# Performance work log

Hardware: AMD Instinct MI355X
Metric: run time of the kernel (lower is better)

Reference implementation:

```python
import jax, jax.numpy as jnp
import numpy as np

NEG_BIG = -1e9

def setup_inputs() -> dict:
    key = jax.random.key(0)
    kq, kk, kv, kwq, kwk, kwv, km = jax.random.split(key, 7)
    B, S, d = 16, 1024, 512
    Q = jax.random.normal(kq, (B, S, d), dtype=jnp.float32)
    K = jax.random.normal(kk, (B, S, d), dtype=jnp.float32)
    V = jax.random.normal(kv, (B, S, d), dtype=jnp.float32)
    # nn.Linear weights [d, d]; torch applies x @ W.T
    WQ = jax.random.normal(kwq, (d, d), dtype=jnp.float32) / np.sqrt(d)
    WK = jax.random.normal(kwk, (d, d), dtype=jnp.float32) / np.sqrt(d)
    WV = jax.random.normal(kwv, (d, d), dtype=jnp.float32) / np.sqrt(d)
    mask = jax.random.randint(km, (B, S), 0, 2, dtype=jnp.int32)
    return {"Q": Q, "K": K, "V": V, "WQ": WQ, "WK": WK, "WV": WV, "mask": mask}


def reference(Q, K, V, WQ, WK, WV, mask):
    d = Q.shape[-1]
    q = jnp.einsum('bsd,ed->bse', Q, WQ)
    k = jnp.einsum('bsd,ed->bse', K, WK)
    v = jnp.einsum('bsd,ed->bse', V, WV)
    scores = jnp.einsum('bqd,bkd->bqk', q, k) / jnp.sqrt(jnp.float32(d))
    attn = jax.nn.softmax(scores, axis=-1)
    # Faithful to original: mask applied AFTER softmax with -1e9 fill
    m = mask[:, None, :]  # [B,1,S] broadcast over query dim
    attn = jnp.where(m == 0, jnp.float32(NEG_BIG), attn)
    out = jnp.einsum('bqk,bkd->bqd', attn, v)
    return (out, attn)
```

## Files before the change

kernel.cpp:

```cpp
#include <hip/hip_runtime.h>
#include <hip/hip_bf16.h>

typedef float f32x4 __attribute__((ext_vector_type(4)));
typedef __bf16 bf16x8 __attribute__((ext_vector_type(8)));
typedef unsigned short u16x8 __attribute__((ext_vector_type(8)));
typedef unsigned short u16x4 __attribute__((ext_vector_type(4)));
typedef int i32x4 __attribute__((ext_vector_type(4)));

#define NEG_BIG_F (-1000000000.0f)
#define SCALE_F 0.044194173824159216f

__device__ __forceinline__ unsigned short f2bf(float f) {
  unsigned int u = __float_as_uint(f);
  u += 0x7FFFu + ((u >> 16) & 1u);
  return (unsigned short)(u >> 16);
}

__device__ __forceinline__ u16x8 cvt8(f32x4 a, f32x4 b) {
  u16x8 r;
  r[0] = f2bf(a[0]); r[1] = f2bf(a[1]); r[2] = f2bf(a[2]); r[3] = f2bf(a[3]);
  r[4] = f2bf(b[0]); r[5] = f2bf(b[1]); r[6] = f2bf(b[2]); r[7] = f2bf(b[3]);
  return r;
}

__device__ __forceinline__ bf16x8 u2b(u16x8 u) {
  union { u16x8 u; bf16x8 b; } c; c.u = u; return c.b;
}

__device__ __forceinline__ void gload16(const void* g, char* l) {
  __builtin_amdgcn_global_load_lds(
      (const __attribute__((address_space(1))) unsigned int*)g,
      (__attribute__((address_space(3))) unsigned int*)l, 16, 0, 0);
}

__global__ __launch_bounds__(256) void cvtW(
    const float* __restrict__ w0, const float* __restrict__ w1,
    const float* __restrict__ w2, unsigned short* __restrict__ out)
{
  const float* src = blockIdx.z == 0 ? w0 : (blockIdx.z == 1 ? w1 : w2);
  unsigned short* dst = out + (size_t)blockIdx.z * 262144;
  const int i = (blockIdx.x * 256 + threadIdx.x) * 8;
  f32x4 a = *(const f32x4*)(src + i);
  f32x4 b = *(const f32x4*)(src + i + 4);
  *(u16x8*)&dst[i] = cvt8(a, b);
}

__global__ __launch_bounds__(256) void proj3(
    const float* __restrict__ Q, const float* __restrict__ Kx,
    const float* __restrict__ V, const unsigned short* __restrict__ wb,
    unsigned short* __restrict__ qb, unsigned short* __restrict__ kb,
    unsigned short* __restrict__ vt)
{
  __shared__ __align__(16) float          Af[2][128][32];
  __shared__ __align__(16) unsigned short Bs[2][128][32];

  const int tid = threadIdx.x;
  const int z = blockIdx.z;
  const float* X = (z == 0) ? Q : (z == 1 ? Kx : V);
  const unsigned short* W = wb + (size_t)z * 262144;
  const int m0 = blockIdx.x * 128, n0 = blockIdx.y * 128;
  const int lane = tid & 63, wave = tid >> 6;
  const int wr = (wave >> 1) * 64, wc = (wave & 1) * 64;
  const int fr = lane & 15, fq = lane >> 4;

  f32x4 acc[4][4] = {};

  const float* gA[4]; char* lA[4];
  #pragma unroll
  for (int i = 0; i < 4; i++) {
    const int c = tid + 256 * i, row = c >> 3, slot = c & 7;
    gA[i] = X + (size_t)(m0 + row) * 512 + ((slot ^ (row & 7)) * 4);
    lA[i] = (char*)&Af[0][0][0] + c * 16;
  }
  const int c1 = 256 + tid;
  const int br0 = tid >> 2, br1 = c1 >> 2;
  const unsigned short* gB0 = W + (size_t)(n0 + br0) * 512 + ((tid & 3) ^ ((br0 >> 1) & 3)) * 8;
  const unsigned short* gB1 = W + (size_t)(n0 + br1) * 512 + ((c1 & 3) ^ ((br1 >> 1) & 3)) * 8;
  char* lB0 = (char*)&Bs[0][0][0] + tid * 16;
  char* lB1 = (char*)&Bs[0][0][0] + c1 * 16;

  #pragma unroll
  for (int i = 0; i < 4; i++) gload16(gA[i], lA[i]);
  gload16(gB0, lB0); gload16(gB1, lB1);
  __syncthreads();

  int cur = 0;
  for (int kt = 0; kt < 512; kt += 32) {
    const int nb = cur ^ 1;
    if (kt + 32 < 512) {
      #pragma unroll
      for (int i = 0; i < 4; i++) gload16(gA[i] + kt + 32, lA[i] + nb * 16384);
      gload16(gB0 + kt + 32, lB0 + nb * 8192);
      gload16(gB1 + kt + 32, lB1 + nb * 8192);
    }
    bf16x8 af[4], bv[4];
    #pragma unroll
    for (int t = 0; t < 4; t++) {
      const int arow = wr + t * 16 + fr;
      const int s0 = (fq * 2) ^ (arow & 7), s1 = (fq * 2 + 1) ^ (arow & 7);
      f32x4 lo = *(const f32x4*)&Af[cur][arow][s0 * 4];
      f32x4 hi = *(const f32x4*)&Af[cur][arow][s1 * 4];
      af[t] = u2b(cvt8(lo, hi));
      const int brow = wc + t * 16 + fr;
      bv[t] = *(const bf16x8*)&Bs[cur][brow][(fq ^ ((brow >> 1) & 3)) * 8];
    }
    #pragma unroll
    for (int mt = 0; mt < 4; mt++)
      #pragma unroll
      for (int nt = 0; nt < 4; nt++)
        acc[mt][nt] = __builtin_amdgcn_mfma_f32_16x16x32_bf16(af[mt], bv[nt], acc[mt][nt], 0, 0, 0);
    __syncthreads();
    cur = nb;
  }

  if (z == 2) {
    #pragma unroll
    for (int mt = 0; mt < 4; mt++)
      #pragma unroll
      for (int nt = 0; nt < 4; nt++)
        #pragma unroll
        for (int rr = 0; rr < 4; rr++) {
          const int m = m0 + wr + mt * 16 + fq * 4 + rr;
          const int n = n0 + wc + nt * 16 + fr;
          vt[((size_t)(m >> 10) * 512 + n) * 1024 + (m & 1023)] = f2bf(acc[mt][nt][rr]);
        }
  } else {
    unsigned short* Y = (z == 0) ? qb : kb;
    #pragma unroll
    for (int mt = 0; mt < 4; mt++)
      #pragma unroll
      for (int nt = 0; nt < 4; nt++)
        #pragma unroll
        for (int rr = 0; rr < 4; rr++) {
          const int m = m0 + wr + mt * 16 + fq * 4 + rr;
          const int n = n0 + wc + nt * 16 + fr;
          Y[(size_t)m * 512 + n] = f2bf(acc[mt][nt][rr]);
        }
  }
}

__global__ __launch_bounds__(256) void score_gemm(
    const unsigned short* __restrict__ qb, const unsigned short* __restrict__ kb,
    float* __restrict__ attn, float* __restrict__ partial)
{
  __shared__ __align__(16) unsigned short As[2][128][32];
  __shared__ __align__(16) unsigned short Bs[2][128][32];

  const int tid = threadIdx.x, z = blockIdx.z;
  const int m0 = blockIdx.x * 128, n0 = blockIdx.y * 128;
  const int lane = tid & 63, wave = tid >> 6;
  const int wr = (wave >> 1) * 64, wc = (wave & 1) * 64;
  const int fr = lane & 15, fq = lane >> 4;

  f32x4 acc[4][4] = {};

  const int c1 = 256 + tid;
  const int br0 = tid >> 2, br1 = c1 >> 2;
  const int sw0 = ((tid & 3) ^ ((br0 >> 1) & 3)) * 8;
  const int sw1 = ((c1 & 3) ^ ((br1 >> 1) & 3)) * 8;
  const unsigned short* gA0 = qb + ((size_t)z * 1024 + m0 + br0) * 512 + sw0;
  const unsigned short* gA1 = qb + ((size_t)z * 1024 + m0 + br1) * 512 + sw1;
  const unsigned short* gB0 = kb + ((size_t)z * 1024 + n0 + br0) * 512 + sw0;
  const unsigned short* gB1 = kb + ((size_t)z * 1024 + n0 + br1) * 512 + sw1;
  char* lA0 = (char*)&As[0][0][0] + tid * 16;
  char* lA1 = (char*)&As[0][0][0] + c1 * 16;
  char* lB0 = (char*)&Bs[0][0][0] + tid * 16;
  char* lB1 = (char*)&Bs[0][0][0] + c1 * 16;

  gload16(gA0, lA0); gload16(gA1, lA1);
  gload16(gB0, lB0); gload16(gB1, lB1);
  __syncthreads();

  int cur = 0;
  for (int kt = 0; kt < 512; kt += 32) {
    const int nb = cur ^ 1;
    if (kt + 32 < 512) {
      gload16(gA0 + kt + 32, lA0 + nb * 8192);
      gload16(gA1 + kt + 32, lA1 + nb * 8192);
      gload16(gB0 + kt + 32, lB0 + nb * 8192);
      gload16(gB1 + kt + 32, lB1 + nb * 8192);
    }
    bf16x8 af[4], bv[4];
    #pragma unroll
    for (int t = 0; t < 4; t++) {
      const int arow = wr + t * 16 + fr;
      const int brow = wc + t * 16 + fr;
      af[t] = *(const bf16x8*)&As[cur][arow][(fq ^ ((arow >> 1) & 3)) * 8];
      bv[t] = *(const bf16x8*)&Bs[cur][brow][(fq ^ ((brow >> 1) & 3)) * 8];
    }
    #pragma unroll
    for (int mt = 0; mt < 4; mt++)
      #pragma unroll
      for (int nt = 0; nt < 4; nt++)
        acc[mt][nt] = __builtin_amdgcn_mfma_f32_16x16x32_bf16(af[mt], bv[nt], acc[mt][nt], 0, 0, 0);
    __syncthreads();
    cur = nb;
  }

  float* Cb = attn + (size_t)z * 1024 * 1024;
  const int slot = blockIdx.y * 2 + (wave & 1);
  #pragma unroll
  for (int mt = 0; mt < 4; mt++) {
    #pragma unroll
    for (int rr = 0; rr < 4; rr++) {
      const int m = m0 + wr + mt * 16 + fq * 4 + rr;
      float e = 0.f;
      #pragma unroll
      for (int nt = 0; nt < 4; nt++) {
        const float sv = acc[mt][nt][rr] * SCALE_F;
        Cb[(size_t)m * 1024 + n0 + wc + nt * 16 + fr] = sv;
        e += __expf(sv);
      }
      e += __shfl_xor(e, 1); e += __shfl_xor(e, 2);
      e += __shfl_xor(e, 4); e += __shfl_xor(e, 8);
      if (fr == 0)
        partial[(size_t)slot * 16384 + z * 1024 + m] = e;
    }
  }
}

__global__ __launch_bounds__(256) void rs_inv(
    const float* __restrict__ partial, float* __restrict__ inv)
{
  const int i = blockIdx.x * 256 + threadIdx.x;
  float s = 0.f;
  #pragma unroll
  for (int p = 0; p < 16; p++) s += partial[(size_t)p * 16384 + i];
  inv[i] = 1.0f / s;
}

__global__ __launch_bounds__(512) void pv_gemm(
    float* __restrict__ attn, const unsigned short* __restrict__ vt,
    const float* __restrict__ inv, const int* __restrict__ mask,
    float* __restrict__ out)
{
  __shared__ __align__(16) unsigned short As[2][64][40];
  __shared__ __align__(16) unsigned short Bs[2][512][32];

  const int tid = threadIdx.x;
  const int bz = blockIdx.z, m0 = blockIdx.x * 64;
  const int lane = tid & 63, wave = tid >> 6;
  const int n0 = wave * 64;
  const int fr = lane & 15, fq = lane >> 4;

  f32x4 acc[4][4] = {};

  const int arow = tid >> 3, acol = (tid & 7) * 4;
  float* arp = attn + ((size_t)bz * 1024 + m0 + arow) * 1024 + acol;
  const float vinv = inv[bz * 1024 + m0 + arow];
  const int* mrow = mask + bz * 1024 + acol;

  const unsigned short* gB[4];
  char* lB[4];
  #pragma unroll
  for (int r = 0; r < 4; r++) {
    const int c = r * 512 + tid;
    const int row = c >> 2;
    gB[r] = vt + ((size_t)bz * 512 + row) * 1024 + ((c & 3) ^ ((row >> 1) & 3)) * 8;
    lB[r] = (char*)&Bs[0][0][0] + c * 16;
  }

  {
    f32x4 s = *(const f32x4*)(arp);
    i32x4 mv = *(const i32x4*)(mrow);
    f32x4 p;
    p[0] = mv[0] ? __expf(s[0]) * vinv : NEG_BIG_F;
    p[1] = mv[1] ? __expf(s[1]) * vinv : NEG_BIG_F;
    p[2] = mv[2] ? __expf(s[2]) * vinv : NEG_BIG_F;
    p[3] = mv[3] ? __expf(s[3]) * vinv : NEG_BIG_F;
    *(f32x4*)(arp) = p;
    u16x4 h;
    h[0] = f2bf(p[0]); h[1] = f2bf(p[1]); h[2] = f2bf(p[2]); h[3] = f2bf(p[3]);
    *(u16x4*)&As[0][arow][acol] = h;
    #pragma unroll
    for (int r = 0; r < 4; r++) gload16(gB[r], lB[r]);
  }
  __syncthreads();

  int cur = 0;
  for (int kt = 0; kt < 1024; kt += 32) {
    const int nb = cur ^ 1;
    f32x4 s; i32x4 mv;
    const bool more = (kt + 32) < 1024;
    if (more) {
      s = *(const f32x4*)(arp + kt + 32);
      mv = *(const i32x4*)(mrow + kt + 32);
      #pragma unroll
      for (int r = 0; r < 4; r++) gload16(gB[r] + kt + 32, lB[r] + nb * 32768);
    }

    bf16x8 af[4], bv[4];
    #pragma unroll
    for (int t = 0; t < 4; t++) {
      af[t] = *(const bf16x8*)&As[cur][t * 16 + fr][fq * 8];
      const int brow = n0 + t * 16 + fr;
      bv[t] = *(const bf16x8*)&Bs[cur][brow][(fq ^ ((brow >> 1) & 3)) * 8];
    }
    #pragma unroll
    for (int mt = 0; mt < 4; mt++)
      #pragma unroll
      for (int nt = 0; nt < 4; nt++)
        acc[mt][nt] = __builtin_amdgcn_mfma_f32_16x16x32_bf16(af[mt], bv[nt], acc[mt][nt], 0, 0, 0);

    if (more) {
      f32x4 p;
      p[0] = mv[0] ? __expf(s[0]) * vinv : NEG_BIG_F;
      p[1] = mv[1] ? __expf(s[1]) * vinv : NEG_BIG_F;
      p[2] = mv[2] ? __expf(s[2]) * vinv : NEG_BIG_F;
      p[3] = mv[3] ? __expf(s[3]) * vinv : NEG_BIG_F;
      *(f32x4*)(arp + kt + 32) = p;
      u16x4 h;
      h[0] = f2bf(p[0]); h[1] = f2bf(p[1]); h[2] = f2bf(p[2]); h[3] = f2bf(p[3]);
      *(u16x4*)&As[nb][arow][acol] = h;
    }
    __syncthreads();
    cur = nb;
  }

  #pragma unroll
  for (int mt = 0; mt < 4; mt++)
    #pragma unroll
    for (int nt = 0; nt < 4; nt++)
      #pragma unroll
      for (int rr = 0; rr < 4; rr++)
        out[((size_t)bz * 1024 + m0 + mt * 16 + fq * 4 + rr) * 512 + n0 + nt * 16 + fr] =
            acc[mt][nt][rr];
}

extern "C" void kernel_launch(void* const* d_in, const int* in_sizes, int n_in,
                              void* d_out, int out_size, void* d_ws, size_t ws_size,
                              hipStream_t stream)
{
  const float* Q  = (const float*)d_in[0];
  const float* Kx = (const float*)d_in[1];
  const float* V  = (const float*)d_in[2];
  const float* WQ = (const float*)d_in[3];
  const float* WK = (const float*)d_in[4];
  const float* WV = (const float*)d_in[5];
  const int* mask = (const int*)d_in[6];

  const int B = 16, S = 1024, D = 512;
  float* out_f  = (float*)d_out;
  float* attn_f = out_f + (size_t)B * S * D;

  unsigned short* qb = (unsigned short*)d_ws;
  unsigned short* kb = qb + (size_t)B * S * D;
  unsigned short* vt = kb + (size_t)B * S * D;
  unsigned short* wb = vt + (size_t)B * S * D;
  float* partial = (float*)(wb + 786432);
  float* inv = partial + 262144;

  cvtW<<<dim3(128, 1, 3), 256, 0, stream>>>(WQ, WK, WV, wb);
  proj3<<<dim3(128, 4, 3), 256, 0, stream>>>(Q, Kx, V, wb, qb, kb, vt);
  score_gemm<<<dim3(8, 8, 16), 256, 0, stream>>>(qb, kb, attn_f, partial);
  rs_inv<<<dim3(64), 256, 0, stream>>>(partial, inv);
  pv_gemm<<<dim3(16, 1, 16), 512, 0, stream>>>(attn_f, vt, inv, mask, out_f);
}
```

Before: 169.1 us.

## Enlarge projection and score GEMM tiles, split V projection to emit V^T directly

The combined projection kernel is split in two. A Q/K projection kernel uses 256x256 tiles with 512 threads; it prefetches the fp32 activations into registers and converts them to bf16 once before the LDS store, instead of every wave re-converting fp32 from LDS. A separate V projection computes W_V·V^T per batch, so the transposed bf16 V is written with coalesced stores instead of scattered ones. The score GEMM moves to 256x256 tiles with explicit waitcnt/barrier pipelining, which raises data reuse per LDS load. The trade-off is higher register and LDS pressure and fewer, larger blocks, which may hurt latency hiding.

```diff
diff --git a/kernel.cpp b/kernel.cpp
--- a/kernel.cpp
+++ b/kernel.cpp
@@ -45,176 +45,285 @@
   *(u16x8*)&dst[i] = cvt8(a, b);
 }
 
-__global__ __launch_bounds__(256) void proj3(
+__global__ __launch_bounds__(512, 2) void projqk(
     const float* __restrict__ Q, const float* __restrict__ Kx,
-    const float* __restrict__ V, const unsigned short* __restrict__ wb,
-    unsigned short* __restrict__ qb, unsigned short* __restrict__ kb,
-    unsigned short* __restrict__ vt)
-{
-  __shared__ __align__(16) float          Af[2][128][32];
-  __shared__ __align__(16) unsigned short Bs[2][128][32];
-
-  const int tid = threadIdx.x;
-  const int z = blockIdx.z;
-  const float* X = (z == 0) ? Q : (z == 1 ? Kx : V);
+    const unsigned short* __restrict__ wb,
+    unsigned short* __restrict__ qb, unsigned short* __restrict__ kb)
+{
+  __shared__ __align__(16) unsigned short As[2][256][32];
+  __shared__ __align__(16) unsigned short Bs[2][256][32];
+
+  const int tid = threadIdx.x, z = blockIdx.z;
+  const float* X = z ? Kx : Q;
   const unsigned short* W = wb + (size_t)z * 262144;
-  const int m0 = blockIdx.x * 128, n0 = blockIdx.y * 128;
+  unsigned short* Y = z ? kb : qb;
+  const int m0 = blockIdx.x * 256, n0 = blockIdx.y * 256;
   const int lane = tid & 63, wave = tid >> 6;
-  const int wr = (wave >> 1) * 64, wc = (wave & 1) * 64;
+  const int wr = (wave >> 2) * 128, wc = (wave & 3) * 64;
   const int fr = lane & 15, fq = lane >> 4;
 
-  f32x4 acc[4][4] = {};
-
-  const float* gA[4]; char* lA[4];
-  #pragma unroll
-  for (int i = 0; i < 4; i++) {
-    const int c = tid + 256 * i, row = c >> 3, slot = c & 7;
-    gA[i] = X + (size_t)(m0 + row) * 512 + ((slot ^ (row & 7)) * 4);
-    lA[i] = (char*)&Af[0][0][0] + c * 16;
-  }
-  const int c1 = 256 + tid;
-  const int br0 = tid >> 2, br1 = c1 >> 2;
-  const unsigned short* gB0 = W + (size_t)(n0 + br0) * 512 + ((tid & 3) ^ ((br0 >> 1) & 3)) * 8;
-  const unsigned short* gB1 = W + (size_t)(n0 + br1) * 512 + ((c1 & 3) ^ ((br1 >> 1) & 3)) * 8;
-  char* lB0 = (char*)&Bs[0][0][0] + tid * 16;
-  char* lB1 = (char*)&Bs[0][0][0] + c1 * 16;
-
-  #pragma unroll
-  for (int i = 0; i < 4; i++) gload16(gA[i], lA[i]);
-  gload16(gB0, lB0); gload16(gB1, lB1);
-  __syncthreads();
+  f32x4 acc[8][4] = {};
+
+  int arow_s[2], aswz_s[2];
+  const float* gAs[2];
+  #pragma unroll
+  for (int i = 0; i < 2; i++) {
+    const int c = tid + 512 * i;
+    arow_s[i] = c >> 2;
+    aswz_s[i] = ((c & 3) ^ ((arow_s[i] >> 1) & 3)) * 8;
+    gAs[i] = X + (size_t)(m0 + arow_s[i]) * 512 + (c & 3) * 8;
+  }
+  const unsigned short* gB[2]; char* lB[2];
+  #pragma unroll
+  for (int i = 0; i < 2; i++) {
+    const int c = tid + 512 * i, row = c >> 2, slot = c & 3;
+    gB[i] = W + (size_t)(n0 + row) * 512 + (slot ^ ((row >> 1) & 3)) * 8;
+    lB[i] = (char*)&Bs[0][0][0] + c * 16;
+  }
+
+  f32x4 pa[2][2];
+  #pragma unroll
+  for (int i = 0; i < 2; i++) {
+    pa[i][0] = *(const f32x4*)(gAs[i]);
+    pa[i][1] = *(const f32x4*)(gAs[i] + 4);
+  }
+  #pragma unroll
+  for (int i = 0; i < 2; i++) gload16(gB[i], lB[i]);
+  #pragma unroll
+  for (int i = 0; i < 2; i++)
+    *(u16x8*)&As[0][arow_s[i]][aswz_s[i]] = cvt8(pa[i][0], pa[i][1]);
 
   int cur = 0;
   for (int kt = 0; kt < 512; kt += 32) {
     const int nb = cur ^ 1;
-    if (kt + 32 < 512) {
-      #pragma unroll
-      for (int i = 0; i < 4; i++) gload16(gA[i] + kt + 32, lA[i] + nb * 16384);
-      gload16(gB0 + kt + 32, lB0 + nb * 8192);
-      gload16(gB1 + kt + 32, lB1 + nb * 8192);
-    }
-    bf16x8 af[4], bv[4];
-    #pragma unroll
-    for (int t = 0; t < 4; t++) {
-      const int arow = wr + t * 16 + fr;
-      const int s0 = (fq * 2) ^ (arow & 7), s1 = (fq * 2 + 1) ^ (arow & 7);
-      f32x4 lo = *(const f32x4*)&Af[cur][arow][s0 * 4];
-      f32x4 hi = *(const f32x4*)&Af[cur][arow][s1 * 4];
-      af[t] = u2b(cvt8(lo, hi));
-      const int brow = wc + t * 16 + fr;
-      bv[t] = *(const bf16x8*)&Bs[cur][brow][(fq ^ ((brow >> 1) & 3)) * 8];
-    }
-    #pragma unroll
-    for (int mt = 0; mt < 4; mt++)
-      #pragma unroll
-      for (int nt = 0; nt < 4; nt++)
-        acc[mt][nt] = __builtin_amdgcn_mfma_f32_16x16x32_bf16(af[mt], bv[nt], acc[mt][nt], 0, 0, 0);
-    __syncthreads();
+    if (kt < 480) {
+      #pragma unroll
+      for (int i = 0; i < 2; i++) {
+        pa[i][0] = *(const f32x4*)(gAs[i] + kt + 32);
+        pa[i][1] = *(const f32x4*)(gAs[i] + kt + 36);
+      }
+      #pragma unroll
+      for (int i = 0; i < 2; i++) gload16(gB[i] + kt + 32, lB[i] + nb * 16384);
+      asm volatile("s_waitcnt vmcnt(6) lgkmcnt(0)" ::: "memory");
+    } else {
+      asm volatile("s_waitcnt vmcnt(0) lgkmcnt(0)" ::: "memory");
+    }
+    __builtin_amdgcn_sched_barrier(0);
+    __builtin_amdgcn_s_barrier();
+
+    bf16x8 bv[4];
+    #pragma unroll
+    for (int nf = 0; nf < 4; nf++) {
+      const int br = wc + nf * 16 + fr;
+      bv[nf] = *(const bf16x8*)&Bs[cur][br][(fq ^ ((br >> 1) & 3)) * 8];
+    }
+    #pragma unroll
+    for (int mf = 0; mf < 8; mf++) {
+      const int ar = wr + mf * 16 + fr;
+      bf16x8 av = *(const bf16x8*)&As[cur][ar][(fq ^ ((ar >> 1) & 3)) * 8];
+      #pragma unroll
+      for (int nf = 0; nf < 4; nf++)
+        acc[mf][nf] = __builtin_amdgcn_mfma_f32_16x16x32_bf16(av, bv[nf], acc[mf][nf], 0, 0, 0);
+    }
+
+    if (kt < 480) {
+      #pragma unroll
+      for (int i = 0; i < 2; i++)
+        *(u16x8*)&As[nb][arow_s[i]][aswz_s[i]] = cvt8(pa[i][0], pa[i][1]);
+    }
+    __builtin_amdgcn_s_barrier();
     cur = nb;
   }
 
-  if (z == 2) {
-    #pragma unroll
-    for (int mt = 0; mt < 4; mt++)
-      #pragma unroll
-      for (int nt = 0; nt < 4; nt++)
-        #pragma unroll
-        for (int rr = 0; rr < 4; rr++) {
-          const int m = m0 + wr + mt * 16 + fq * 4 + rr;
-          const int n = n0 + wc + nt * 16 + fr;
-          vt[((size_t)(m >> 10) * 512 + n) * 1024 + (m & 1023)] = f2bf(acc[mt][nt][rr]);
-        }
-  } else {
-    unsigned short* Y = (z == 0) ? qb : kb;
-    #pragma unroll
-    for (int mt = 0; mt < 4; mt++)
-      #pragma unroll
-      for (int nt = 0; nt < 4; nt++)
-        #pragma unroll
-        for (int rr = 0; rr < 4; rr++) {
-          const int m = m0 + wr + mt * 16 + fq * 4 + rr;
-          const int n = n0 + wc + nt * 16 + fr;
-          Y[(size_t)m * 512 + n] = f2bf(acc[mt][nt][rr]);
-        }
-  }
-}
-
-__global__ __launch_bounds__(256) void score_gemm(
-    const unsigned short* __restrict__ qb, const unsigned short* __restrict__ kb,
-    float* __restrict__ attn, float* __restrict__ partial)
+  #pragma unroll
+  for (int mf = 0; mf < 8; mf++)
+    #pragma unroll
+    for (int nf = 0; nf < 4; nf++)
+      #pragma unroll
+      for (int rr = 0; rr < 4; rr++) {
+        const int m = m0 + wr + mf * 16 + fq * 4 + rr;
+        const int n = n0 + wc + nf * 16 + fr;
+        Y[(size_t)m * 512 + n] = f2bf(acc[mf][nf][rr]);
+      }
+}
+
+__global__ __launch_bounds__(512, 2) void projv(
+    const float* __restrict__ V, const unsigned short* __restrict__ wv,
+    unsigned short* __restrict__ vt)
 {
   __shared__ __align__(16) unsigned short As[2][128][32];
-  __shared__ __align__(16) unsigned short Bs[2][128][32];
-
-  const int tid = threadIdx.x, z = blockIdx.z;
-  const int m0 = blockIdx.x * 128, n0 = blockIdx.y * 128;
+  __shared__ __align__(16) unsigned short Bs[2][256][32];
+
+  const int tid = threadIdx.x;
+  const int m0 = blockIdx.x * 128, n0 = blockIdx.y * 256, b = blockIdx.z;
   const int lane = tid & 63, wave = tid >> 6;
-  const int wr = (wave >> 1) * 64, wc = (wave & 1) * 64;
+  const int wr = (wave >> 2) * 64, wc = (wave & 3) * 64;
   const int fr = lane & 15, fq = lane >> 4;
 
   f32x4 acc[4][4] = {};
 
-  const int c1 = 256 + tid;
-  const int br0 = tid >> 2, br1 = c1 >> 2;
-  const int sw0 = ((tid & 3) ^ ((br0 >> 1) & 3)) * 8;
-  const int sw1 = ((c1 & 3) ^ ((br1 >> 1) & 3)) * 8;
-  const unsigned short* gA0 = qb + ((size_t)z * 1024 + m0 + br0) * 512 + sw0;
-  const unsigned short* gA1 = qb + ((size_t)z * 1024 + m0 + br1) * 512 + sw1;
-  const unsigned short* gB0 = kb + ((size_t)z * 1024 + n0 + br0) * 512 + sw0;
-  const unsigned short* gB1 = kb + ((size_t)z * 1024 + n0 + br1) * 512 + sw1;
-  char* lA0 = (char*)&As[0][0][0] + tid * 16;
-  char* lA1 = (char*)&As[0][0][0] + c1 * 16;
-  char* lB0 = (char*)&Bs[0][0][0] + tid * 16;
-  char* lB1 = (char*)&Bs[0][0][0] + c1 * 16;
-
-  gload16(gA0, lA0); gload16(gA1, lA1);
-  gload16(gB0, lB0); gload16(gB1, lB1);
-  __syncthreads();
+  const int ar_s = tid >> 2, aslot = tid & 3;
+  const unsigned short* gA = wv + (size_t)(m0 + ar_s) * 512 + (aslot ^ ((ar_s >> 1) & 3)) * 8;
+  char* lA = (char*)&As[0][0][0] + tid * 16;
+
+  int brow_s[2], bswz_s[2];
+  const float* gBs[2];
+  #pragma unroll
+  for (int i = 0; i < 2; i++) {
+    const int c = tid + 512 * i;
+    brow_s[i] = c >> 2;
+    bswz_s[i] = ((c & 3) ^ ((brow_s[i] >> 1) & 3)) * 8;
+    gBs[i] = V + ((size_t)b * 1024 + n0 + brow_s[i]) * 512 + (c & 3) * 8;
+  }
+
+  f32x4 pb[2][2];
+  #pragma unroll
+  for (int i = 0; i < 2; i++) {
+    pb[i][0] = *(const f32x4*)(gBs[i]);
+    pb[i][1] = *(const f32x4*)(gBs[i] + 4);
+  }
+  gload16(gA, lA);
+  #pragma unroll
+  for (int i = 0; i < 2; i++)
+    *(u16x8*)&Bs[0][brow_s[i]][bswz_s[i]] = cvt8(pb[i][0], pb[i][1]);
 
   int cur = 0;
   for (int kt = 0; kt < 512; kt += 32) {
     const int nb = cur ^ 1;
-    if (kt + 32 < 512) {
-      gload16(gA0 + kt + 32, lA0 + nb * 8192);
-      gload16(gA1 + kt + 32, lA1 + nb * 8192);
-      gload16(gB0 + kt + 32, lB0 + nb * 8192);
-      gload16(gB1 + kt + 32, lB1 + nb * 8192);
-    }
-    bf16x8 af[4], bv[4];
-    #pragma unroll
-    for (int t = 0; t < 4; t++) {
-      const int arow = wr + t * 16 + fr;
-      const int brow = wc + t * 16 + fr;
-      af[t] = *(const bf16x8*)&As[cur][arow][(fq ^ ((arow >> 1) & 3)) * 8];
-      bv[t] = *(const bf16x8*)&Bs[cur][brow][(fq ^ ((brow >> 1) & 3)) * 8];
-    }
-    #pragma unroll
-    for (int mt = 0; mt < 4; mt++)
-      #pragma unroll
-      for (int nt = 0; nt < 4; nt++)
-        acc[mt][nt] = __builtin_amdgcn_mfma_f32_16x16x32_bf16(af[mt], bv[nt], acc[mt][nt], 0, 0, 0);
-    __syncthreads();
+    if (kt < 480) {
+      #pragma unroll
+      for (int i = 0; i < 2; i++) {
+        pb[i][0] = *(const f32x4*)(gBs[i] + kt + 32);
+        pb[i][1] = *(const f32x4*)(gBs[i] + kt + 36);
+      }
+      gload16(gA + kt + 32, lA + nb * 8192);
+      asm volatile("s_waitcnt vmcnt(5) lgkmcnt(0)" ::: "memory");
+    } else {
+      asm volatile("s_waitcnt vmcnt(0) lgkmcnt(0)" ::: "memory");
+    }
+    __builtin_amdgcn_sched_barrier(0);
+    __builtin_amdgcn_s_barrier();
+
+    bf16x8 av[4], bv[4];
+    #pragma unroll
+    for (int mf = 0; mf < 4; mf++) {
+      const int ar = wr + mf * 16 + fr;
+      av[mf] = *(const bf16x8*)&As[cur][ar][(fq ^ ((ar >> 1) & 3)) * 8];
+    }
+    #pragma unroll
+    for (int nf = 0; nf < 4; nf++) {
+      const int br = wc + nf * 16 + fr;
+      bv[nf] = *(const bf16x8*)&Bs[cur][br][(fq ^ ((br >> 1) & 3)) * 8];
+    }
+    #pragma unroll
+    for (int mf = 0; mf < 4; mf++)
+      #pragma unroll
+      for (int nf = 0; nf < 4; nf++)
+        acc[mf][nf] = __builtin_amdgcn_mfma_f32_16x16x32_bf16(av[mf], bv[nf], acc[mf][nf], 0, 0, 0);
+
+    if (kt < 480) {
+      #pragma unroll
+      for (int i = 0; i < 2; i++)
+        *(u16x8*)&Bs[nb][brow_s[i]][bswz_s[i]] = cvt8(pb[i][0], pb[i][1]);
+    }
+    __builtin_amdgcn_s_barrier();
     cur = nb;
   }
 
-  float* Cb = attn + (size_t)z * 1024 * 1024;
-  const int slot = blockIdx.y * 2 + (wave & 1);
-  #pragma unroll
-  for (int mt = 0; mt < 4; mt++) {
+  #pragma unroll
+  for (int mf = 0; mf < 4; mf++)
+    #pragma unroll
+    for (int nf = 0; nf < 4; nf++)
+      #pragma unroll
+      for (int rr = 0; rr < 4; rr++) {
+        const int e = m0 + wr + mf * 16 + fq * 4 + rr;
+        const int s = n0 + wc + nf * 16 + fr;
+        vt[((size_t)b * 512 + e) * 1024 + s] = f2bf(acc[mf][nf][rr]);
+      }
+}
+
+__global__ __launch_bounds__(512, 2) void score256(
+    const unsigned short* __restrict__ qb, const unsigned short* __restrict__ kb,
+    float* __restrict__ attn, float* __restrict__ partial)
+{
+  __shared__ __align__(16) unsigned short As[2][256][32];
+  __shared__ __align__(16) unsigned short Bs[2][256][32];
+
+  const int tid = threadIdx.x, bz = blockIdx.z;
+  const int m0 = blockIdx.x * 256, n0 = blockIdx.y * 256;
+  const int lane = tid & 63, wave = tid >> 6;
+  const int wr = (wave >> 2) * 128, wc = (wave & 3) * 64;
+  const int fr = lane & 15, fq = lane >> 4;
+
+  f32x4 acc[8][4] = {};
+
+  const unsigned short* gA[2]; char* lA[2];
+  const unsigned short* gB[2]; char* lB[2];
+  #pragma unroll
+  for (int i = 0; i < 2; i++) {
+    const int c = tid + 512 * i, row = c >> 2, slot = c & 3;
+    const int sw = (slot ^ ((row >> 1) & 3)) * 8;
+    gA[i] = qb + ((size_t)bz * 1024 + m0 + row) * 512 + sw;
+    gB[i] = kb + ((size_t)bz * 1024 + n0 + row) * 512 + sw;
+    lA[i] = (char*)&As[0][0][0] + c * 16;
+    lB[i] = (char*)&Bs[0][0][0] + c * 16;
+  }
+
+  #pragma unroll
+  for (int i = 0; i < 2; i++) { gload16(gA[i], lA[i]); gload16(gB[i], lB[i]); }
+
+  int cur = 0;
+  for (int kt = 0; kt < 512; kt += 32) {
+    const int nb = cur ^ 1;
+    if (kt < 480) {
+      #pragma unroll
+      for (int i = 0; i < 2; i++) {
+        gload16(gA[i] + kt + 32, lA[i] + nb * 16384);
+        gload16(gB[i] + kt + 32, lB[i] + nb * 16384);
+      }
+      asm volatile("s_waitcnt vmcnt(4) lgkmcnt(0)" ::: "memory");
+    } else {
+      asm volatile("s_waitcnt vmcnt(0) lgkmcnt(0)" ::: "memory");
+    }
+    __builtin_amdgcn_sched_barrier(0);
+    __builtin_amdgcn_s_barrier();
+
+    bf16x8 bv[4];
+    #pragma unroll
+    for (int nf = 0; nf < 4; nf++) {
+      const int br = wc + nf * 16 + fr;
+      bv[nf] = *(const bf16x8*)&Bs[cur][br][(fq ^ ((br >> 1) & 3)) * 8];
+    }
+    #pragma unroll
+    for (int mf = 0; mf < 8; mf++) {
+      const int ar = wr + mf * 16 + fr;
+      bf16x8 av = *(const bf16x8*)&As[cur][ar][(fq ^ ((ar >> 1) & 3)) * 8];
+      #pragma unroll
+      for (int nf = 0; nf < 4; nf++)
+        acc[mf][nf] = __builtin_amdgcn_mfma_f32_16x16x32_bf16(av, bv[nf], acc[mf][nf], 0, 0, 0);
+    }
+    __builtin_amdgcn_s_barrier();
+    cur = nb;
+  }
+
+  float* Cb = attn + (size_t)bz * 1024 * 1024;
+  const int slot = blockIdx.y * 4 + (wave & 3);
+  #pragma unroll
+  for (int mf = 0; mf < 8; mf++) {
     #pragma unroll
     for (int rr = 0; rr < 4; rr++) {
-      const int m = m0 + wr + mt * 16 + fq * 4 + rr;
+      const int m = m0 + wr + mf * 16 + fq * 4 + rr;
       float e = 0.f;
       #pragma unroll
-      for (int nt = 0; nt < 4; nt++) {
-        const float sv = acc[mt][nt][rr] * SCALE_F;
-        Cb[(size_t)m * 1024 + n0 + wc + nt * 16 + fr] = sv;
+      for (int nf = 0; nf < 4; nf++) {
+        const float sv = acc[mf][nf][rr] * SCALE_F;
+        Cb[(size_t)m * 1024 + n0 + wc + nf * 16 + fr] = sv;
         e += __expf(sv);
       }
       e += __shfl_xor(e, 1); e += __shfl_xor(e, 2);
       e += __shfl_xor(e, 4); e += __shfl_xor(e, 8);
       if (fr == 0)
-        partial[(size_t)slot * 16384 + z * 1024 + m] = e;
+        partial[(size_t)slot * 16384 + bz * 1024 + m] = e;
     }
   }
 }
@@ -351,8 +460,9 @@
   float* inv = partial + 262144;
 
   cvtW<<<dim3(128, 1, 3), 256, 0, stream>>>(WQ, WK, WV, wb);
-  proj3<<<dim3(128, 4, 3), 256, 0, stream>>>(Q, Kx, V, wb, qb, kb, vt);
-  score_gemm<<<dim3(8, 8, 16), 256, 0, stream>>>(qb, kb, attn_f, partial);
+  projqk<<<dim3(64, 2, 2), 512, 0, stream>>>(Q, Kx, wb, qb, kb);
+  projv<<<dim3(4, 4, 16), 512, 0, stream>>>(V, wb + 524288, vt);
+  score256<<<dim3(4, 4, 16), 512, 0, stream>>>(qb, kb, attn_f, partial);
   rs_inv<<<dim3(64), 256, 0, stream>>>(partial, inv);
   pv_gemm<<<dim3(16, 1, 16), 512, 0, stream>>>(attn_f, vt, inv, mask, out_f);
 }
```

Measured after the change: 163.5 us. 3.3% less time.
